# Kernel tuning notes

Hardware: AMD Instinct MI355X
Metric: run time of the kernel (lower is better)

The kernel has to match this reference:

```python
import jax, jax.numpy as jnp
import numpy as np

N = 100000   # nodes
E = 640000   # edges
H = 8        # attention heads
C = 16       # hidden_channels (per-head out dim)
IN = 4       # in_channels
G = 64       # graphs in the batch
NE = 2       # num_experts
HC = H * C   # 128 = concat feature width
SLOPE = 0.2  # GATConv leaky_relu negative slope


def _p(k, shape):
    return 0.1 * jax.random.normal(k, shape, jnp.float32)


def setup_inputs() -> dict:
    key = jax.random.key(0)
    ks = jax.random.split(key, 32)
    inp = {
        "x": jax.random.normal(ks[0], (N, IN), jnp.float32),
        "edge_index": jax.random.randint(ks[1], (2, E), 0, N),
        "edge_attr": jax.random.normal(ks[2], (E, 1), jnp.float32),
        "batch": jnp.sort(jax.random.randint(ks[3], (N,), 0, G)),
    }
    i = 4
    for l, d in zip((1, 2, 3), (IN, HC, HC)):
        inp[f"w{l}"] = _p(ks[i], (d, HC)); i += 1      # node lin
        inp[f"as{l}"] = _p(ks[i], (H, C)); i += 1      # att_src
        inp[f"ad{l}"] = _p(ks[i], (H, C)); i += 1      # att_dst
        inp[f"we{l}"] = _p(ks[i], (1, HC)); i += 1     # lin_edge
        inp[f"ae{l}"] = _p(ks[i], (H, C)); i += 1      # att_edge
        inp[f"b{l}"] = jnp.zeros((HC,), jnp.float32)
    inp["fw1"] = _p(ks[i], (HC, 4 * C)); inp["fb1"] = jnp.zeros((4 * C,), jnp.float32)
    inp["fw2"] = _p(ks[i + 1], (4 * C, NE)); inp["fb2"] = jnp.zeros((NE,), jnp.float32)
    return inp


def gat_layer(x, src, dst, eattr, w, a_s, a_d, we, a_e, b):
    """PyG GATConv (concat=True, edge_dim=1): gather-attend-segment_softmax-scatter."""
    n = x.shape[0]
    h = (x @ w).reshape(n, H, C)                       # [N,H,C]
    alpha_src = jnp.sum(h * a_s, axis=-1)              # [N,H]
    alpha_dst = jnp.sum(h * a_d, axis=-1)              # [N,H]
    ef = (eattr @ we).reshape(-1, H, C)                # [E,H,C]
    alpha_e = jnp.sum(ef * a_e, axis=-1)               # [E,H]
    alpha = jax.nn.leaky_relu(alpha_src[src] + alpha_dst[dst] + alpha_e, SLOPE)
    # segment softmax over incoming edges of each dst node
    m = jax.lax.stop_gradient(jax.ops.segment_max(alpha, dst, num_segments=n))
    m = jnp.where(jnp.isfinite(m), m, 0.0)
    ex = jnp.exp(alpha - m[dst])
    den = jax.ops.segment_sum(ex, dst, num_segments=n)
    alpha = ex / (den[dst] + 1e-16)
    out = jax.ops.segment_sum(h[src] * alpha[:, :, None], dst, num_segments=n)
    return out.reshape(n, HC) + b


def add_self_loops_mean(src, dst, eattr, n):
    """add_self_loops(fill_value='mean'): self-loop attr = mean of incoming edge attrs."""
    cnt = jax.ops.segment_sum(jnp.ones(src.shape, eattr.dtype), dst, num_segments=n)
    loop = jax.ops.segment_sum(eattr, dst, num_segments=n) / jnp.maximum(cnt, 1.0)[:, None]
    idx = jnp.arange(n, dtype=src.dtype)
    return (jnp.concatenate([src, idx]), jnp.concatenate([dst, idx]),
            jnp.concatenate([eattr, loop], axis=0))


def reference(x, edge_index, edge_attr, batch,
              w1, as1, ad1, we1, ae1, b1,
              w2, as2, ad2, we2, ae2, b2,
              w3, as3, ad3, we3, ae3, b3,
              fw1, fb1, fw2, fb2):
    src, dst = edge_index[0], edge_index[1]
    # conv1: add_self_loops=False
    h = jax.nn.relu(gat_layer(x, src, dst, edge_attr, w1, as1, ad1, we1, ae1, b1))
    # conv2/conv3: default add_self_loops=True with fill_value='mean'
    s2, d2, e2 = add_self_loops_mean(src, dst, edge_attr, x.shape[0])
    h = jax.nn.relu(gat_layer(h, s2, d2, e2, w2, as2, ad2, we2, ae2, b2))
    h = jax.nn.relu(gat_layer(h, s2, d2, e2, w3, as3, ad3, we3, ae3, b3))
    # global mean pool over `batch`
    gsum = jax.ops.segment_sum(h, batch, num_segments=G)
    cnt = jax.ops.segment_sum(jnp.ones((h.shape[0],), h.dtype), batch, num_segments=G)
    emb = gsum / jnp.maximum(cnt, 1.0)[:, None]
    gh = jax.nn.relu(emb @ fw1 + fb1)
    return gh @ fw2 + fb2
```

## Files before the change

### kernel.cpp

```cpp
#include <hip/hip_runtime.h>
#include <hip/hip_bf16.h>
#include <math.h>

#define NHEAD 8
#define CDIM 16
#define HCDIM 128
#define NGRAPH 64
#define WEXT 144
#define SWPAD 136

typedef __attribute__((ext_vector_type(8))) short short8;
typedef __attribute__((ext_vector_type(4))) float f32x4;
typedef __attribute__((ext_vector_type(2))) float f32x2;

static __device__ __forceinline__ unsigned short f2bf(float f) {
    unsigned u = __float_as_uint(f);
    unsigned r = (u + 0x7FFF + ((u >> 16) & 1)) >> 16;
    return (unsigned short)r;
}
static __device__ __forceinline__ float bf2f(unsigned short s) {
    return __uint_as_float(((unsigned)s) << 16);
}
static __device__ __forceinline__ unsigned char f2fp8(float v) {
    int r = __builtin_amdgcn_cvt_pk_fp8_f32(v, v, 0, false);
    return (unsigned char)(r & 0xff);
}
static __device__ __forceinline__ float fp82f(int x) {
    f32x2 t = __builtin_amdgcn_cvt_pk_f32_fp8(x, false);
    return t[0];
}


__global__ void setup0(int* __restrict__ deg,
                       float* __restrict__ gsum,
                       const float* __restrict__ w2, const float* __restrict__ w3,
                       unsigned short* __restrict__ wt2, unsigned short* __restrict__ wt3,
                       const float* __restrict__ we1, const float* __restrict__ ae1,
                       const float* __restrict__ we2, const float* __restrict__ ae2,
                       const float* __restrict__ we3, const float* __restrict__ ae3,
                       float* __restrict__ kc,
                       const float* __restrict__ as2, const float* __restrict__ ad2,
                       const float* __restrict__ as3, const float* __restrict__ ad3,
                       const float* __restrict__ w1,
                       const float* __restrict__ as1, const float* __restrict__ ad1,
                       float* __restrict__ wastab, float* __restrict__ wadtab,
                       const int* __restrict__ batch, int* __restrict__ gstart, int n) {
    int i = blockIdx.x * 256 + threadIdx.x;
    if (i < n) deg[i] = 0;
    if (i < NGRAPH * HCDIM) gsum[i] = 0.f;
    if (i < WEXT * HCDIM) {
        int nn = i >> 7, k = i & 127;
        float v2, v3;
        if (nn < HCDIM) {
            v2 = w2[k * HCDIM + nn];
            v3 = w3[k * HCDIM + nn];
        } else if (nn < HCDIM + NHEAD) {
            int h = nn - HCDIM;
            float s2 = 0.f, s3 = 0.f;
#pragma unroll
            for (int c = 0; c < CDIM; ++c) {
                s2 += w2[k * HCDIM + h * CDIM + c] * as2[h * CDIM + c];
                s3 += w3[k * HCDIM + h * CDIM + c] * as3[h * CDIM + c];
            }
            v2 = s2; v3 = s3;
        } else {
            int h = nn - HCDIM - NHEAD;
            float s2 = 0.f, s3 = 0.f;
#pragma unroll
            for (int c = 0; c < CDIM; ++c) {
                s2 += w2[k * HCDIM + h * CDIM + c] * ad2[h * CDIM + c];
                s3 += w3[k * HCDIM + h * CDIM + c] * ad3[h * CDIM + c];
            }
            v2 = s2; v3 = s3;
        }
        wt2[nn * HCDIM + k] = f2bf(v2);
        wt3[nn * HCDIM + k] = f2bf(v3);
    }
    if (i < 24) {
        int l = i >> 3, h = i & 7;
        const float* we = (l == 0) ? we1 : ((l == 1) ? we2 : we3);
        const float* ae = (l == 0) ? ae1 : ((l == 1) ? ae2 : ae3);
        float s = 0.f;
        for (int c = 0; c < CDIM; ++c) s += we[h * CDIM + c] * ae[h * CDIM + c];
        kc[i] = s;
    }
    if (i >= 18560 && i <= 18560 + NGRAPH) {
        int g = i - 18560;
        int lo = 0, hi = n;
        while (lo < hi) {
            int mid = (lo + hi) >> 1;
            if (batch[mid] < g) lo = mid + 1; else hi = mid;
        }
        gstart[g] = lo;
    }
    if (i >= 18700 && i < 18732) {
        int t = i - 18700;
        int k = t >> 3, h = t & 7;
        float ss = 0.f, sd = 0.f;
#pragma unroll
        for (int c = 0; c < CDIM; ++c) {
            ss += w1[k * HCDIM + h * CDIM + c] * as1[h * CDIM + c];
            sd += w1[k * HCDIM + h * CDIM + c] * ad1[h * CDIM + c];
        }
        wastab[t] = ss;
        wadtab[t] = sd;
    }
}

__global__ void count_deg(const int* __restrict__ dst, int* __restrict__ deg,
                          int* __restrict__ erank, int E) {
    int e = blockIdx.x * 256 + threadIdx.x;
    if (e >= E) return;
    erank[e] = atomicAdd(&deg[dst[e]], 1);
}

__global__ __launch_bounds__(512) void block_sum(const int* __restrict__ deg,
                                                 int* __restrict__ bsum, int n) {
    __shared__ int s[512];
    int i = blockIdx.x * 512 + threadIdx.x;
    s[threadIdx.x] = (i < n) ? deg[i] : 0;
    __syncthreads();
    for (int off = 256; off > 0; off >>= 1) {
        if (threadIdx.x < off) s[threadIdx.x] += s[threadIdx.x + off];
        __syncthreads();
    }
    if (threadIdx.x == 0) bsum[blockIdx.x] = s[0];
}

__global__ __launch_bounds__(512) void scan_final2(const int* __restrict__ deg,
                                                   const int* __restrict__ bsum, int nb,
                                                   int* __restrict__ eoff, int n) {
    __shared__ int ls[512];
    __shared__ int s[512];
    const int t = threadIdx.x;
    ls[t] = (t < nb) ? bsum[t] : 0;
    int i = blockIdx.x * 512 + t;
    s[t] = (i < n) ? deg[i] : 0;
    __syncthreads();
    for (int off = 1; off < 512; off <<= 1) {
        int a1 = (t >= off) ? ls[t - off] : 0;
        int a2 = (t >= off) ? s[t - off] : 0;
        __syncthreads();
        ls[t] += a1; s[t] += a2;
        __syncthreads();
    }
    int base = (blockIdx.x > 0) ? ls[blockIdx.x - 1] : 0;
    if (i < n) eoff[i + 1] = base + s[t];
    if (i == 0) eoff[0] = 0;
}

__global__ void scatter_edges(const int* __restrict__ src, const int* __restrict__ dst,
                              const float* __restrict__ eattr,
                              const int* __restrict__ eoff,
                              const int* __restrict__ erank,
                              unsigned* __restrict__ epack, int E) {
    int e = blockIdx.x * 256 + threadIdx.x;
    if (e >= E) return;
    int p = eoff[dst[e]] + erank[e];
    epack[p] = ((unsigned)src[e] & 0xFFFFFFu) | ((unsigned)f2fp8(eattr[e]) << 24);
}


__global__ __launch_bounds__(256) void gat_aggregate1(
    const float* __restrict__ x,
    const unsigned* __restrict__ epack,
    const int*   __restrict__ eoff,
    const float* __restrict__ w1,
    const float* __restrict__ wastab,
    const float* __restrict__ wadtab,
    const float* __restrict__ kc,
    const float* __restrict__ bias,
    unsigned char* __restrict__ out8,
    int n) {
    const int lane = threadIdx.x & 63;
    const int l16 = lane & 15;
    int nid = ((blockIdx.x * 256 + threadIdx.x) >> 6) * 4 + (lane >> 4);
    if (nid >= n) return;
    const int h = l16 >> 1;
    const int c0 = l16 * 8;

    float was0 = wastab[0 * NHEAD + h], was1_ = wastab[1 * NHEAD + h];
    float was2 = wastab[2 * NHEAD + h], was3 = wastab[3 * NHEAD + h];
    float wad0 = wadtab[0 * NHEAD + h], wad1_ = wadtab[1 * NHEAD + h];
    float wad2 = wadtab[2 * NHEAD + h], wad3 = wadtab[3 * NHEAD + h];

    f32x4 xd = *(const f32x4*)(x + (((unsigned)nid) << 2));
    const float adst_h = xd[0] * wad0 + xd[1] * wad1_ + xd[2] * wad2 + xd[3] * wad3;
    const float k_h = kc[h];
    const int e0 = eoff[nid], e1 = eoff[nid + 1];

    float den = 0.f;
    f32x4 acc4 = (f32x4){0.f, 0.f, 0.f, 0.f};

    if (e0 < e1) {
        unsigned ep[4];
#pragma unroll
        for (int j = 0; j < 4; ++j) {
            int idx = e0 + j; idx = (idx < e1) ? idx : (e1 - 1);
            ep[j] = epack[idx];
        }
        for (int base = e0; base < e1; base += 4) {
            unsigned epn[4];
#pragma unroll
            for (int j = 0; j < 4; ++j) {
                int idx = base + 4 + j; idx = (idx < e1) ? idx : (e1 - 1);
                epn[j] = epack[idx];
            }
            f32x4 xs[4];
#pragma unroll
            for (int j = 0; j < 4; ++j)
                xs[j] = *(const f32x4*)(x + ((ep[j] & 0xFFFFFFu) << 2));
#pragma unroll
            for (int j = 0; j < 4; ++j) {
                bool valid = (base + j < e1);
                float as_e = xs[j][0] * was0 + xs[j][1] * was1_ +
                             xs[j][2] * was2 + xs[j][3] * was3;
                float ea = fp82f((int)(ep[j] >> 24));
                float a = as_e + adst_h + ea * k_h;
                a = (a > 0.f) ? a : 0.2f * a;
                float w = valid ? __expf(a) : 0.f;
                den += w;
                acc4 += xs[j] * w;
            }
#pragma unroll
            for (int j = 0; j < 4; ++j) ep[j] = epn[j];
        }
    }

    float inv = 1.f / (den + 1e-16f);
    float oc[8];
#pragma unroll
    for (int c = 0; c < 8; ++c) {
        float v = acc4[0] * w1[0 * HCDIM + c0 + c] + acc4[1] * w1[1 * HCDIM + c0 + c] +
                  acc4[2] * w1[2 * HCDIM + c0 + c] + acc4[3] * w1[3 * HCDIM + c0 + c];
        oc[c] = fmaxf(v * inv + bias[c0 + c], 0.f);
    }
    int w0 = __builtin_amdgcn_cvt_pk_fp8_f32(oc[0], oc[1], 0, false);
    w0 = __builtin_amdgcn_cvt_pk_fp8_f32(oc[2], oc[3], w0, true);
    int w1p = __builtin_amdgcn_cvt_pk_fp8_f32(oc[4], oc[5], 0, false);
    w1p = __builtin_amdgcn_cvt_pk_fp8_f32(oc[6], oc[7], w1p, true);
    *(uint2*)(out8 + ((long)nid << 7) + c0) = make_uint2((unsigned)w0, (unsigned)w1p);
}


__global__ __launch_bounds__(256) void gemm_mfma(const unsigned char* __restrict__ A8,
                                                 const unsigned short* __restrict__ Wt,
                                                 unsigned char* __restrict__ Y8,
                                                 float* __restrict__ adstn, int n) {
    __shared__ unsigned short sW[WEXT][SWPAD];
    for (int i = threadIdx.x; i < WEXT * 16; i += 256) {
        int r = i >> 4, c = (i & 15) << 3;
        *(short8*)&sW[r][c] = *(const short8*)(Wt + r * HCDIM + c);
    }
    __syncthreads();

    const int wave = threadIdx.x >> 6;
    const int lane = threadIdx.x & 63;
    const int quad = lane >> 4;
    const int l16  = lane & 15;
    const int rowbase = (blockIdx.x * 8 + wave * 2) * 16;

    f32x4 acc[2][9];
#pragma unroll
    for (int r = 0; r < 2; ++r)
#pragma unroll
        for (int t = 0; t < 9; ++t) acc[r][t] = (f32x4){0.f, 0.f, 0.f, 0.f};

#pragma unroll
    for (int kb = 0; kb < HCDIM; kb += 32) {
        short8 a[2];
#pragma unroll
        for (int r = 0; r < 2; ++r) {
            int row = rowbase + r * 16 + l16;
            row = (row < n) ? row : (n - 1);
            uint2 a8v = *(const uint2*)(A8 + (long)row * HCDIM + kb + quad * 8);
            f32x2 q0 = __builtin_amdgcn_cvt_pk_f32_fp8((int)a8v.x, false);
            f32x2 q1 = __builtin_amdgcn_cvt_pk_f32_fp8((int)a8v.x, true);
            f32x2 q2 = __builtin_amdgcn_cvt_pk_f32_fp8((int)a8v.y, false);
            f32x2 q3 = __builtin_amdgcn_cvt_pk_f32_fp8((int)a8v.y, true);
            a[r][0] = (short)f2bf(q0[0]); a[r][1] = (short)f2bf(q0[1]);
            a[r][2] = (short)f2bf(q1[0]); a[r][3] = (short)f2bf(q1[1]);
            a[r][4] = (short)f2bf(q2[0]); a[r][5] = (short)f2bf(q2[1]);
            a[r][6] = (short)f2bf(q3[0]); a[r][7] = (short)f2bf(q3[1]);
        }
#pragma unroll
        for (int nt = 0; nt < 9; ++nt) {
            short8 b = *(const short8*)(&sW[nt * 16 + l16][kb + quad * 8]);
#pragma unroll
            for (int r = 0; r < 2; ++r)
                acc[r][nt] = __builtin_amdgcn_mfma_f32_16x16x32_bf16(a[r], b, acc[r][nt], 0, 0, 0);
        }
    }

#pragma unroll
    for (int r = 0; r < 2; ++r) {
#pragma unroll
        for (int reg = 0; reg < 4; ++reg) {
            int row = rowbase + r * 16 + quad * 4 + reg;
            if (row < n) {
                unsigned char* yp = Y8 + (long)row * HCDIM + l16;
#pragma unroll
                for (int nt = 0; nt < 8; ++nt) yp[nt * 16] = f2fp8(acc[r][nt][reg]);
                if (l16 >= 8) adstn[row * NHEAD + (l16 - 8)] = acc[r][8][reg];
            }
        }
    }
}


__global__ __launch_bounds__(256) void gat_aggregate(
    const unsigned char* __restrict__ h8,
    const float* __restrict__ adst,
    const float* __restrict__ asw,
    const unsigned* __restrict__ epack,
    const int*   __restrict__ eoff,
    const float* __restrict__ kc,
    const float* __restrict__ bias,
    void* __restrict__ out,
    int n, int out_fp8) {
    const int lane = threadIdx.x & 63;
    const int l16 = lane & 15;
    int nid = ((blockIdx.x * 256 + threadIdx.x) >> 6) * 4 + (lane >> 4);
    if (nid >= n) return;
    const int h = l16 >> 1;
    const int c0 = l16 * 8;

    const float* asrow = asw + h * CDIM + (l16 & 1) * 8;
    const f32x2 wp0 = *(const f32x2*)(asrow + 0);
    const f32x2 wp1 = *(const f32x2*)(asrow + 2);
    const f32x2 wp2 = *(const f32x2*)(asrow + 4);
    const f32x2 wp3 = *(const f32x2*)(asrow + 6);

    const float adst_h = adst[nid * NHEAD + h];
    const float k_h = kc[h];
    const int e0 = eoff[nid], e1 = eoff[nid + 1];

    float den = 0.f, sume = 0.f;
    f32x2 acc[4];
#pragma unroll
    for (int p = 0; p < 4; ++p) acc[p] = (f32x2){0.f, 0.f};

    if (e0 < e1) {
        unsigned ep[4];
#pragma unroll
        for (int j = 0; j < 4; ++j) {
            int idx = e0 + j; idx = (idx < e1) ? idx : (e1 - 1);
            ep[j] = epack[idx];
        }
        for (int base = e0; base < e1; base += 4) {
            unsigned epn[4];
#pragma unroll
            for (int j = 0; j < 4; ++j) {
                int idx = base + 4 + j; idx = (idx < e1) ? idx : (e1 - 1);
                epn[j] = epack[idx];
            }
            uint2 hv[4];
#pragma unroll
            for (int j = 0; j < 4; ++j)
                hv[j] = *(const uint2*)(h8 + ((long)(ep[j] & 0xFFFFFFu) << 7) + c0);
#pragma unroll
            for (int j = 0; j < 4; ++j) {
                bool valid = (base + j < e1);
                f32x2 p0 = __builtin_amdgcn_cvt_pk_f32_fp8((int)hv[j].x, false);
                f32x2 p1 = __builtin_amdgcn_cvt_pk_f32_fp8((int)hv[j].x, true);
                f32x2 p2 = __builtin_amdgcn_cvt_pk_f32_fp8((int)hv[j].y, false);
                f32x2 p3 = __builtin_amdgcn_cvt_pk_f32_fp8((int)hv[j].y, true);
                f32x2 ds = p0 * wp0 + p1 * wp1 + p2 * wp2 + p3 * wp3;
                float part = ds[0] + ds[1];
                float as_e = part + __shfl_xor(part, 1, 64);
                float ea = fp82f((int)(ep[j] >> 24));
                float a = as_e + adst_h + ea * k_h;
                a = (a > 0.f) ? a : 0.2f * a;
                float w = valid ? __expf(a) : 0.f;
                sume += valid ? ea : 0.f;
                den += w;
                acc[0] += p0 * w;
                acc[1] += p1 * w;
                acc[2] += p2 * w;
                acc[3] += p3 * w;
            }
#pragma unroll
            for (int j = 0; j < 4; ++j) ep[j] = epn[j];
        }
    }

    {
        float fl = sume / fmaxf((float)(e1 - e0), 1.f);
        uint2 hv = *(const uint2*)(h8 + ((long)(unsigned)nid << 7) + c0);
        f32x2 p0 = __builtin_amdgcn_cvt_pk_f32_fp8((int)hv.x, false);
        f32x2 p1 = __builtin_amdgcn_cvt_pk_f32_fp8((int)hv.x, true);
        f32x2 p2 = __builtin_amdgcn_cvt_pk_f32_fp8((int)hv.y, false);
        f32x2 p3 = __builtin_amdgcn_cvt_pk_f32_fp8((int)hv.y, true);
        f32x2 ds = p0 * wp0 + p1 * wp1 + p2 * wp2 + p3 * wp3;
        float part = ds[0] + ds[1];
        float as_self = part + __shfl_xor(part, 1, 64);
        float a = as_self + adst_h + fl * k_h;
        a = (a > 0.f) ? a : 0.2f * a;
        float w = __expf(a);
        den += w;
        acc[0] += p0 * w;
        acc[1] += p1 * w;
        acc[2] += p2 * w;
        acc[3] += p3 * w;
    }

    float inv = 1.f / (den + 1e-16f);
    float oc[8];
#pragma unroll
    for (int c = 0; c < 8; ++c)
        oc[c] = fmaxf(acc[c >> 1][c & 1] * inv + bias[c0 + c], 0.f);
    if (out_fp8) {
        int w0 = __builtin_amdgcn_cvt_pk_fp8_f32(oc[0], oc[1], 0, false);
        w0 = __builtin_amdgcn_cvt_pk_fp8_f32(oc[2], oc[3], w0, true);
        int w1p = __builtin_amdgcn_cvt_pk_fp8_f32(oc[4], oc[5], 0, false);
        w1p = __builtin_amdgcn_cvt_pk_fp8_f32(oc[6], oc[7], w1p, true);
        *(uint2*)((unsigned char*)out + ((long)nid << 7) + c0) =
            make_uint2((unsigned)w0, (unsigned)w1p);
    } else {
        short8 o;
#pragma unroll
        for (int c = 0; c < 8; ++c) o[c] = (short)f2bf(oc[c]);
        *(short8*)((unsigned short*)out + (long)nid * HCDIM + c0) = o;
    }
}


__global__ __launch_bounds__(128) void pool_seg(const unsigned short* __restrict__ H,
                                                const int* __restrict__ gstart,
                                                float* __restrict__ gsum) {
    const int c = threadIdx.x;
    const int g = blockIdx.x >> 3;
    const int chunk = blockIdx.x & 7;
    int s0 = gstart[g], s1 = gstart[g + 1];
    int len = s1 - s0;
    if (len <= 0) return;
    int cl = (len + 7) >> 3;
    int i0 = s0 + chunk * cl;
    int i1 = min(i0 + cl, s1);
    if (i0 >= i1) return;
    float acc = 0.f;
    int i = i0;
    for (; i + 4 <= i1; i += 4) {
        float v0 = bf2f(H[(long)i * HCDIM + c]);
        float v1 = bf2f(H[(long)(i + 1) * HCDIM + c]);
        float v2 = bf2f(H[(long)(i + 2) * HCDIM + c]);
        float v3 = bf2f(H[(long)(i + 3) * HCDIM + c]);
        acc += (v0 + v1) + (v2 + v3);
    }
    for (; i < i1; ++i) acc += bf2f(H[(long)i * HCDIM + c]);
    atomicAdd(&gsum[g * HCDIM + c], acc);
}

__global__ __launch_bounds__(64) void mlp_kernel(const float* __restrict__ gsum,
                                                 const int* __restrict__ gstart,
                                                 const float* __restrict__ fw1,
                                                 const float* __restrict__ fb1,
                                                 const float* __restrict__ fw2,
                                                 const float* __restrict__ fb2,
                                                 float* __restrict__ out) {
    const int g = blockIdx.x;
    const int j = threadIdx.x;
    __shared__ float emb[HCDIM];
    __shared__ float gh[64];
    int cnt = gstart[g + 1] - gstart[g];
    float invc = 1.f / fmaxf((float)cnt, 1.f);
    emb[j] = gsum[g * HCDIM + j] * invc;
    emb[j + 64] = gsum[g * HCDIM + 64 + j] * invc;
    __syncthreads();
    float a = fb1[j];
    for (int k = 0; k < HCDIM; ++k) a += emb[k] * fw1[k * 64 + j];
    gh[j] = fmaxf(a, 0.f);
    __syncthreads();
    if (j < 2) {
        float o = fb2[j];
        for (int k = 0; k < 64; ++k) o += gh[k] * fw2[k * 2 + j];
        out[g * 2 + j] = o;
    }
}


extern "C" void kernel_launch(void* const* d_in, const int* in_sizes, int n_in,
                              void* d_out, int out_size, void* d_ws, size_t ws_size,
                              hipStream_t stream) {
    const float* x     = (const float*)d_in[0];
    const int*   eidx  = (const int*)d_in[1];
    const float* eattr = (const float*)d_in[2];
    const int*   batch = (const int*)d_in[3];
    const float* w1  = (const float*)d_in[4];
    const float* as1 = (const float*)d_in[5];
    const float* ad1 = (const float*)d_in[6];
    const float* we1 = (const float*)d_in[7];
    const float* ae1 = (const float*)d_in[8];
    const float* b1  = (const float*)d_in[9];
    const float* w2  = (const float*)d_in[10];
    const float* as2 = (const float*)d_in[11];
    const float* ad2 = (const float*)d_in[12];
    const float* we2 = (const float*)d_in[13];
    const float* ae2 = (const float*)d_in[14];
    const float* b2  = (const float*)d_in[15];
    const float* w3  = (const float*)d_in[16];
    const float* as3 = (const float*)d_in[17];
    const float* ad3 = (const float*)d_in[18];
    const float* we3 = (const float*)d_in[19];
    const float* ae3 = (const float*)d_in[20];
    const float* b3  = (const float*)d_in[21];
    const float* fw1 = (const float*)d_in[22];
    const float* fb1 = (const float*)d_in[23];
    const float* fw2 = (const float*)d_in[24];
    const float* fb2 = (const float*)d_in[25];

    const int N = in_sizes[3];
    const int E = in_sizes[2];
    const int* src = eidx;
    const int* dst = eidx + E;

    char* p = (char*)d_ws;
    auto alloc = [&](size_t bytes) {
        void* r = (void*)p;
        p += (bytes + 255) & ~(size_t)255;
        return r;
    };
    unsigned char*  A8  = (unsigned char*)alloc((size_t)N * HCDIM);
    unsigned char*  B8  = (unsigned char*)alloc((size_t)N * HCDIM);
    unsigned short* Cbf = (unsigned short*)alloc((size_t)N * HCDIM * 2);
    float* adstA  = (float*)alloc((size_t)N * NHEAD * 4);
    float* adstB  = (float*)alloc((size_t)N * NHEAD * 4);
    int*   deg    = (int*)alloc((size_t)N * 4);
    int*   eoff   = (int*)alloc((size_t)(N + 1) * 4);
    int*   erank  = (int*)alloc((size_t)E * 4);
    unsigned* epack = (unsigned*)alloc((size_t)E * 4);
    int*   bsum   = (int*)alloc(((size_t)(N + 511) / 512) * 4);
    float* kc     = (float*)alloc(24 * 4);
    int*   gstart = (int*)alloc((NGRAPH + 1) * 4);
    float* gsum   = (float*)alloc(NGRAPH * HCDIM * 4);
    float* wastab = (float*)alloc(32 * 4);
    float* wadtab = (float*)alloc(32 * 4);
    unsigned short* wt2 = (unsigned short*)alloc(WEXT * HCDIM * 2);
    unsigned short* wt3 = (unsigned short*)alloc(WEXT * HCDIM * 2);

    const int NB = (N + 255) / 256;
    const int NB512 = (N + 511) / 512;
    const int EB = (E + 255) / 256;
    const int AGG_BLOCKS = (((N + 3) / 4) * 64 + 255) / 256;
    const int GEMM_BLOCKS = (N + 127) / 128;

    setup0<<<NB, 256, 0, stream>>>(deg, gsum,
                                   w2, w3, wt2, wt3,
                                   we1, ae1, we2, ae2, we3, ae3, kc,
                                   as2, ad2, as3, ad3,
                                   w1, as1, ad1, wastab, wadtab,
                                   batch, gstart, N);
    count_deg<<<EB, 256, 0, stream>>>(dst, deg, erank, E);
    block_sum<<<NB512, 512, 0, stream>>>(deg, bsum, N);
    scan_final2<<<NB512, 512, 0, stream>>>(deg, bsum, NB512, eoff, N);
    scatter_edges<<<EB, 256, 0, stream>>>(src, dst, eattr, eoff, erank, epack, E);

    gat_aggregate1<<<AGG_BLOCKS, 256, 0, stream>>>(x, epack, eoff, w1, wastab, wadtab,
                                                   kc + 0, b1, B8, N);
    gemm_mfma<<<GEMM_BLOCKS, 256, 0, stream>>>(B8, wt2, A8, adstB, N);
    gat_aggregate<<<AGG_BLOCKS, 256, 0, stream>>>(A8, adstB, as2, epack, eoff,
                                                  kc + 8, b2, (void*)B8, N, 1);
    gemm_mfma<<<GEMM_BLOCKS, 256, 0, stream>>>(B8, wt3, A8, adstA, N);
    gat_aggregate<<<AGG_BLOCKS, 256, 0, stream>>>(A8, adstA, as3, epack, eoff,
                                                  kc + 16, b3, (void*)Cbf, N, 0);

    pool_seg<<<NGRAPH * 8, 128, 0, stream>>>(Cbf, gstart, gsum);
    mlp_kernel<<<NGRAPH, 64, 0, stream>>>(gsum, gstart, fw1, fb1, fw2, fb2, (float*)d_out);
}
```

Before: 300.4 us.

## Fuse degree scan into single-pass lookback kernel and store final layer in fp8

Replaces the two-kernel block-sum plus scan with one kernel where each block publishes its total through a flag array and sums the totals of earlier blocks by spinning on those flags. This removes one launch and its dependency. The final GAT layer now writes fp8 instead of bf16, which halves the bytes written and then read by the pooling kernel but lowers precision. The lookback depends on earlier blocks making progress, which holds here because the block count is small (196).

```diff
diff --git a/kernel.cpp b/kernel.cpp
--- a/kernel.cpp
+++ b/kernel.cpp
@@ -44,7 +44,8 @@
                        const float* __restrict__ w1,
                        const float* __restrict__ as1, const float* __restrict__ ad1,
                        float* __restrict__ wastab, float* __restrict__ wadtab,
-                       const int* __restrict__ batch, int* __restrict__ gstart, int n) {
+                       const int* __restrict__ batch, int* __restrict__ gstart,
+                       int* __restrict__ bflag, int n) {
     int i = blockIdx.x * 256 + threadIdx.x;
     if (i < n) deg[i] = 0;
     if (i < NGRAPH * HCDIM) gsum[i] = 0.f;
@@ -105,6 +106,7 @@
         wastab[t] = ss;
         wadtab[t] = sd;
     }
+    if (i >= 19000 && i < 19256) bflag[i - 19000] = 0;
 }
 
 __global__ void count_deg(const int* __restrict__ dst, int* __restrict__ deg,
@@ -114,37 +116,35 @@
     erank[e] = atomicAdd(&deg[dst[e]], 1);
 }
 
-__global__ __launch_bounds__(512) void block_sum(const int* __restrict__ deg,
-                                                 int* __restrict__ bsum, int n) {
+__global__ __launch_bounds__(512) void scan_lookback(const int* __restrict__ deg,
+                                                     int* __restrict__ bflag,
+                                                     int* __restrict__ eoff, int n) {
     __shared__ int s[512];
-    int i = blockIdx.x * 512 + threadIdx.x;
-    s[threadIdx.x] = (i < n) ? deg[i] : 0;
-    __syncthreads();
-    for (int off = 256; off > 0; off >>= 1) {
-        if (threadIdx.x < off) s[threadIdx.x] += s[threadIdx.x + off];
-        __syncthreads();
-    }
-    if (threadIdx.x == 0) bsum[blockIdx.x] = s[0];
-}
-
-__global__ __launch_bounds__(512) void scan_final2(const int* __restrict__ deg,
-                                                   const int* __restrict__ bsum, int nb,
-                                                   int* __restrict__ eoff, int n) {
     __shared__ int ls[512];
-    __shared__ int s[512];
     const int t = threadIdx.x;
-    ls[t] = (t < nb) ? bsum[t] : 0;
-    int i = blockIdx.x * 512 + t;
+    const int b = blockIdx.x;
+    int i = b * 512 + t;
     s[t] = (i < n) ? deg[i] : 0;
     __syncthreads();
     for (int off = 1; off < 512; off <<= 1) {
-        int a1 = (t >= off) ? ls[t - off] : 0;
-        int a2 = (t >= off) ? s[t - off] : 0;
+        int a = (t >= off) ? s[t - off] : 0;
         __syncthreads();
-        ls[t] += a1; s[t] += a2;
+        s[t] += a;
         __syncthreads();
     }
-    int base = (blockIdx.x > 0) ? ls[blockIdx.x - 1] : 0;
+    if (t == 0) atomicExch(&bflag[b], s[511] + 1);
+    ls[t] = 0;
+    if (t < b) {
+        int v;
+        do { v = atomicAdd(&bflag[t], 0); } while (v == 0);
+        ls[t] = v - 1;
+    }
+    __syncthreads();
+    for (int off = 256; off > 0; off >>= 1) {
+        if (t < off) ls[t] += ls[t + off];
+        __syncthreads();
+    }
+    int base = ls[0];
     if (i < n) eoff[i + 1] = base + s[t];
     if (i == 0) eoff[0] = 0;
 }
@@ -316,8 +316,8 @@
     const int*   __restrict__ eoff,
     const float* __restrict__ kc,
     const float* __restrict__ bias,
-    void* __restrict__ out,
-    int n, int out_fp8) {
+    unsigned char* __restrict__ out8,
+    int n) {
     const int lane = threadIdx.x & 63;
     const int l16 = lane & 15;
     int nid = ((blockIdx.x * 256 + threadIdx.x) >> 6) * 4 + (lane >> 4);
@@ -409,23 +409,15 @@
 #pragma unroll
     for (int c = 0; c < 8; ++c)
         oc[c] = fmaxf(acc[c >> 1][c & 1] * inv + bias[c0 + c], 0.f);
-    if (out_fp8) {
-        int w0 = __builtin_amdgcn_cvt_pk_fp8_f32(oc[0], oc[1], 0, false);
-        w0 = __builtin_amdgcn_cvt_pk_fp8_f32(oc[2], oc[3], w0, true);
-        int w1p = __builtin_amdgcn_cvt_pk_fp8_f32(oc[4], oc[5], 0, false);
-        w1p = __builtin_amdgcn_cvt_pk_fp8_f32(oc[6], oc[7], w1p, true);
-        *(uint2*)((unsigned char*)out + ((long)nid << 7) + c0) =
-            make_uint2((unsigned)w0, (unsigned)w1p);
-    } else {
-        short8 o;
-#pragma unroll
-        for (int c = 0; c < 8; ++c) o[c] = (short)f2bf(oc[c]);
-        *(short8*)((unsigned short*)out + (long)nid * HCDIM + c0) = o;
-    }
-}
-
-
-__global__ __launch_bounds__(128) void pool_seg(const unsigned short* __restrict__ H,
+    int w0 = __builtin_amdgcn_cvt_pk_fp8_f32(oc[0], oc[1], 0, false);
+    w0 = __builtin_amdgcn_cvt_pk_fp8_f32(oc[2], oc[3], w0, true);
+    int w1p = __builtin_amdgcn_cvt_pk_fp8_f32(oc[4], oc[5], 0, false);
+    w1p = __builtin_amdgcn_cvt_pk_fp8_f32(oc[6], oc[7], w1p, true);
+    *(uint2*)(out8 + ((long)nid << 7) + c0) = make_uint2((unsigned)w0, (unsigned)w1p);
+}
+
+
+__global__ __launch_bounds__(128) void pool_seg(const unsigned char* __restrict__ H8,
                                                 const int* __restrict__ gstart,
                                                 float* __restrict__ gsum) {
     const int c = threadIdx.x;
@@ -441,13 +433,13 @@
     float acc = 0.f;
     int i = i0;
     for (; i + 4 <= i1; i += 4) {
-        float v0 = bf2f(H[(long)i * HCDIM + c]);
-        float v1 = bf2f(H[(long)(i + 1) * HCDIM + c]);
-        float v2 = bf2f(H[(long)(i + 2) * HCDIM + c]);
-        float v3 = bf2f(H[(long)(i + 3) * HCDIM + c]);
+        float v0 = fp82f((int)H8[(long)i * HCDIM + c]);
+        float v1 = fp82f((int)H8[(long)(i + 1) * HCDIM + c]);
+        float v2 = fp82f((int)H8[(long)(i + 2) * HCDIM + c]);
+        float v3 = fp82f((int)H8[(long)(i + 3) * HCDIM + c]);
         acc += (v0 + v1) + (v2 + v3);
     }
-    for (; i < i1; ++i) acc += bf2f(H[(long)i * HCDIM + c]);
+    for (; i < i1; ++i) acc += fp82f((int)H8[(long)i * HCDIM + c]);
     atomicAdd(&gsum[g * HCDIM + c], acc);
 }
 
@@ -522,14 +514,13 @@
     };
     unsigned char*  A8  = (unsigned char*)alloc((size_t)N * HCDIM);
     unsigned char*  B8  = (unsigned char*)alloc((size_t)N * HCDIM);
-    unsigned short* Cbf = (unsigned short*)alloc((size_t)N * HCDIM * 2);
     float* adstA  = (float*)alloc((size_t)N * NHEAD * 4);
     float* adstB  = (float*)alloc((size_t)N * NHEAD * 4);
     int*   deg    = (int*)alloc((size_t)N * 4);
     int*   eoff   = (int*)alloc((size_t)(N + 1) * 4);
     int*   erank  = (int*)alloc((size_t)E * 4);
     unsigned* epack = (unsigned*)alloc((size_t)E * 4);
-    int*   bsum   = (int*)alloc(((size_t)(N + 511) / 512) * 4);
+    int*   bflag  = (int*)alloc(256 * 4);
     float* kc     = (float*)alloc(24 * 4);
     int*   gstart = (int*)alloc((NGRAPH + 1) * 4);
     float* gsum   = (float*)alloc(NGRAPH * HCDIM * 4);
@@ -549,21 +540,20 @@
                                    we1, ae1, we2, ae2, we3, ae3, kc,
                                    as2, ad2, as3, ad3,
                                    w1, as1, ad1, wastab, wadtab,
-                                   batch, gstart, N);
+                                   batch, gstart, bflag, N);
     count_deg<<<EB, 256, 0, stream>>>(dst, deg, erank, E);
-    block_sum<<<NB512, 512, 0, stream>>>(deg, bsum, N);
-    scan_final2<<<NB512, 512, 0, stream>>>(deg, bsum, NB512, eoff, N);
+    scan_lookback<<<NB512, 512, 0, stream>>>(deg, bflag, eoff, N);
     scatter_edges<<<EB, 256, 0, stream>>>(src, dst, eattr, eoff, erank, epack, E);
 
     gat_aggregate1<<<AGG_BLOCKS, 256, 0, stream>>>(x, epack, eoff, w1, wastab, wadtab,
                                                    kc + 0, b1, B8, N);
     gemm_mfma<<<GEMM_BLOCKS, 256, 0, stream>>>(B8, wt2, A8, adstB, N);
     gat_aggregate<<<AGG_BLOCKS, 256, 0, stream>>>(A8, adstB, as2, epack, eoff,
-                                                  kc + 8, b2, (void*)B8, N, 1);
+                                                  kc + 8, b2, B8, N);
     gemm_mfma<<<GEMM_BLOCKS, 256, 0, stream>>>(B8, wt3, A8, adstA, N);
     gat_aggregate<<<AGG_BLOCKS, 256, 0, stream>>>(A8, adstA, as3, epack, eoff,
-                                                  kc + 16, b3, (void*)Cbf, N, 0);
-
-    pool_seg<<<NGRAPH * 8, 128, 0, stream>>>(Cbf, gstart, gsum);
+                                                  kc + 16, b3, B8, N);
+
+    pool_seg<<<NGRAPH * 8, 128, 0, stream>>>(B8, gstart, gsum);
     mlp_kernel<<<NGRAPH, 64, 0, stream>>>(gsum, gstart, fw1, fb1, fw2, fb2, (float*)d_out);
 }
```

Result: no change. 302.1 us (+0.6%).
